# Kernel tuning notes

Hardware: AMD Instinct MI355X
Metric: run time of the kernel (lower is better)

## Reference

```python
import jax, jax.numpy as jnp
import numpy as np

N, E, D, L = 50000, 800000, 128, 2
EPS = 1e-7

def _logmap0(y):
    # Poincare ball (c=1) logmap at origin: artanh(||y||) * y / ||y||
    n = jnp.linalg.norm(y, axis=-1, keepdims=True)
    nc = jnp.clip(n, EPS, 1.0 - 1e-5)
    return jnp.arctanh(nc) * y / jnp.maximum(n, EPS)

def _expmap0(u):
    # Poincare ball (c=1) expmap at origin: tanh(||u||) * u / ||u||
    n = jnp.linalg.norm(u, axis=-1, keepdims=True)
    return jnp.tanh(n) * u / jnp.maximum(n, EPS)

def _l2norm(x):
    # F.normalize(p=2, dim=1)
    return x / jnp.maximum(jnp.linalg.norm(x, axis=1, keepdims=True), 1e-12)

def setup_inputs() -> dict:
    key = jax.random.key(0)
    ks = jax.random.split(key, 12)
    src = jax.random.randint(ks[0], (E,), 0, N)
    dst = jax.random.randint(ks[1], (E,), 0, N)
    e_emb = jax.random.normal(ks[2], (N, D), jnp.float32)
    b_emb = jax.random.normal(ks[3], (N, D), jnp.float32) * 0.1  # inside Poincare ball
    s_emb = jax.random.normal(ks[4], (N, D), jnp.float32)
    sc = 0.05
    eW = jax.random.normal(ks[5], (L, D, D), jnp.float32) * sc
    eB = jax.random.normal(ks[6], (L, D), jnp.float32) * sc
    bW = jax.random.normal(ks[7], (L, D, D), jnp.float32) * sc
    bB = jax.random.normal(ks[8], (L, D), jnp.float32) * sc
    sW = jax.random.normal(ks[9], (L, D, D), jnp.float32) * sc
    sB = jax.random.normal(ks[10], (L, D), jnp.float32) * sc
    return dict(e_emb=e_emb, b_emb=b_emb, s_emb=s_emb, eW=eW, eB=eB,
                bW=bW, bB=bB, sW=sW, sB=sB, src=src, dst=dst)

def reference(e_emb, b_emb, s_emb, eW, eB, bW, bB, sW, sB, src, dst):
    n_nodes = e_emb.shape[0]
    ones_e = jnp.ones(src.shape[0], jnp.float32)
    in_deg = jax.ops.segment_sum(ones_e, dst, num_segments=n_nodes)
    out_deg = jax.ops.segment_sum(ones_e, src, num_segments=n_nodes)
    # DGL GraphConv norm='both': D_out^{-1/2} (sum over in-neighbors) D_in^{-1/2}
    norm_out = jnp.where(out_deg > 0, out_deg ** -0.5, 0.0)[:, None]
    norm_in = jnp.where(in_deg > 0, in_deg ** -0.5, 0.0)[:, None]
    inv_in = jnp.where(in_deg > 0, 1.0 / in_deg, 0.0)[:, None]  # mean reduce

    def agg_sum(h):
        return jax.ops.segment_sum(h[src], dst, num_segments=n_nodes)

    for l in range(L):
        # Euclidean branch: GraphConv(norm='both') then LeakyReLU(0.2)
        h = agg_sum(e_emb * norm_out) * norm_in
        e_emb = jax.nn.leaky_relu(h @ eW[l].T + eB[l], negative_slope=0.2)
        # Hyperbolic branch: logmap0 -> Linear -> neighbor mean -> expmap0
        tan_b = _logmap0(b_emb) @ bW[l].T + bB[l]
        b_emb = _expmap0(agg_sum(tan_b) * inv_in)
        # Spherical branch: normalize -> Linear -> neighbor mean -> normalize
        tan_s = _l2norm(s_emb) @ sW[l].T + sB[l]
        s_emb = _l2norm(agg_sum(tan_s) * inv_in)
    return (e_emb, b_emb, s_emb)
```

## Files before the change

kernel.cpp:

```cpp
#include <hip/hip_runtime.h>
#include <math.h>

#define DD 128
#define PSTRIDE 384

typedef _Float16 half8 __attribute__((ext_vector_type(8)));
typedef float floatx4 __attribute__((ext_vector_type(4)));

__device__ __forceinline__ float g16_sum(float x) {
#pragma unroll
  for (int m = 8; m >= 1; m >>= 1) x += __shfl_xor(x, m, 64);
  return x;
}
__device__ __forceinline__ int wave_sum_i(int x) {
#pragma unroll
  for (int m = 32; m >= 1; m >>= 1) x += __shfl_xor(x, m, 64);
  return x;
}

__global__ void deg_wcvt_kernel(const int* __restrict__ src, const int* __restrict__ dst,
                                int* __restrict__ out_deg8, int* __restrict__ in_deg8,
                                int E, int N,
                                const float* __restrict__ eW, const float* __restrict__ bW,
                                const float* __restrict__ sW, _Float16* __restrict__ Wh, int nW,
                                int DB) {
  int bx = blockIdx.x;
  if (bx < DB) {
    int e = bx * 256 + threadIdx.x;
    if (e < E) {
      int h = ((bx << 2) + (threadIdx.x >> 6)) & 7;
      atomicAdd(&out_deg8[h * N + src[e]], 1);
      atomicAdd(&in_deg8[h * N + dst[e]], 1);
    }
  } else {
    int i = (bx - DB) * 256 + threadIdx.x;
    if (i < nW) {
      Wh[i]          = (_Float16)eW[i];
      Wh[i + nW]     = (_Float16)bW[i];
      Wh[i + 2 * nW] = (_Float16)sW[i];
    }
  }
}

__global__ void norms_psum_kernel(const int* __restrict__ in_deg8, const int* __restrict__ out_deg8,
                                  int* __restrict__ in_deg, float* __restrict__ norm_in,
                                  float* __restrict__ norm_out, float* __restrict__ inv_in,
                                  int* __restrict__ part, int N) {
  __shared__ int wsum[4];
  int t = threadIdx.x, lane = t & 63, w = t >> 6;
  int i = blockIdx.x * 256 + t;
  int di = 0;
  if (i < N) {
    int dq = 0;
#pragma unroll
    for (int h = 0; h < 8; ++h) {
      di += in_deg8[h * N + i];
      dq += out_deg8[h * N + i];
    }
    in_deg[i] = di;
    norm_in[i]  = di > 0 ? 1.0f / sqrtf((float)di) : 0.0f;
    norm_out[i] = dq > 0 ? 1.0f / sqrtf((float)dq) : 0.0f;
    inv_in[i]   = di > 0 ? 1.0f / (float)di : 0.0f;
  }
  int s = wave_sum_i(di);
  if (lane == 0) wsum[w] = s;
  __syncthreads();
  if (t == 0) part[blockIdx.x] = wsum[0] + wsum[1] + wsum[2] + wsum[3];
}

__global__ void part_scan_kernel(int* __restrict__ part, int nb) {
  __shared__ int wsum[4];
  int t = threadIdx.x, lane = t & 63, w = t >> 6;
  int x = (t < nb) ? part[t] : 0;
  int v = x;
#pragma unroll
  for (int off = 1; off < 64; off <<= 1) {
    int y = __shfl_up(v, off, 64);
    if (lane >= off) v += y;
  }
  if (lane == 63) wsum[w] = v;
  __syncthreads();
  int base = 0;
  for (int j = 0; j < w; ++j) base += wsum[j];
  if (t < nb) part[t] = base + v - x;
}

__global__ void local_scan_kernel(const int* __restrict__ deg, const int* __restrict__ part,
                                  int* __restrict__ row_off, int N, int E) {
  __shared__ int wsum[4];
  int t = threadIdx.x, lane = t & 63, w = t >> 6;
  int i = blockIdx.x * 256 + t;
  int x = (i < N) ? deg[i] : 0;
  int v = x;
#pragma unroll
  for (int off = 1; off < 64; off <<= 1) {
    int y = __shfl_up(v, off, 64);
    if (lane >= off) v += y;
  }
  if (lane == 63) wsum[w] = v;
  __syncthreads();
  int base = 0;
  for (int j = 0; j < w; ++j) base += wsum[j];
  if (i < N) row_off[i] = part[blockIdx.x] + base + v - x;
  if (blockIdx.x == 0 && t == 0) row_off[N] = E;
}

__device__ __forceinline__ void gemm0_tile(int part, int rb, const float* __restrict__ A,
                                           const _Float16* __restrict__ Wh,
                                           const float* __restrict__ Bb,
                                           _Float16* __restrict__ Q, int N) {
  int t = threadIdx.x, lane = t & 63, w = t >> 6;
  int m = lane & 15, quad = lane >> 4, c0 = w * 32;
  int rbase = rb * 64;
  _Float16* Qo = Q + part * DD;
  half8 bf[2][4];
#pragma unroll
  for (int tj = 0; tj < 2; ++tj)
#pragma unroll
    for (int kk = 0; kk < 4; ++kk)
      bf[tj][kk] = *(const half8*)&Wh[(c0 + tj * 16 + m) * DD + kk * 32 + quad * 8];
  float bias0 = 0.f, bias1 = 0.f;
  if (part) { bias0 = Bb[c0 + m]; bias1 = Bb[c0 + 16 + m]; }
#pragma unroll
  for (int r = 0; r < 4; ++r) {
    int row0 = r * 16;
    int arow = rbase + row0 + m; if (arow >= N) arow = N - 1;
    const float* Ap = A + (size_t)arow * DD;
    half8 af[4];
    float nsq = 0.f;
#pragma unroll
    for (int kk = 0; kk < 4; ++kk) {
      float4 x0 = *(const float4*)&Ap[kk * 32 + quad * 8];
      float4 x1 = *(const float4*)&Ap[kk * 32 + quad * 8 + 4];
      if (part)
        nsq += x0.x * x0.x + x0.y * x0.y + x0.z * x0.z + x0.w * x0.w +
               x1.x * x1.x + x1.y * x1.y + x1.z * x1.z + x1.w * x1.w;
      half8 a;
      a[0] = (_Float16)x0.x; a[1] = (_Float16)x0.y; a[2] = (_Float16)x0.z; a[3] = (_Float16)x0.w;
      a[4] = (_Float16)x1.x; a[5] = (_Float16)x1.y; a[6] = (_Float16)x1.z; a[7] = (_Float16)x1.w;
      af[kk] = a;
    }
    float fr = 1.f;
    if (part) {
      nsq += __shfl_xor(nsq, 16, 64);
      nsq += __shfl_xor(nsq, 32, 64);
      float n = sqrtf(nsq);
      if (part == 1) {
        float nc = fminf(fmaxf(n, 1e-7f), 1.0f - 1e-5f);
        fr = atanhf(nc) / fmaxf(n, 1e-7f);
      } else {
        fr = 1.0f / fmaxf(n, 1e-12f);
      }
    }
    floatx4 acc0 = {0.f, 0.f, 0.f, 0.f}, acc1 = {0.f, 0.f, 0.f, 0.f};
#pragma unroll
    for (int kk = 0; kk < 4; ++kk) {
      acc0 = __builtin_amdgcn_mfma_f32_16x16x32_f16(af[kk], bf[0][kk], acc0, 0, 0, 0);
      acc1 = __builtin_amdgcn_mfma_f32_16x16x32_f16(af[kk], bf[1][kk], acc1, 0, 0, 0);
    }
    int vrow = rbase + row0 + quad * 4;
#pragma unroll
    for (int reg = 0; reg < 4; ++reg) {
      int v = vrow + reg;
      float fs = part ? __shfl(fr, quad * 4 + reg, 64) : 1.f;
      if (v < N) {
        Qo[(size_t)v * PSTRIDE + c0 + m]      = (_Float16)(acc0[reg] * fs + bias0);
        Qo[(size_t)v * PSTRIDE + c0 + 16 + m] = (_Float16)(acc1[reg] * fs + bias1);
      }
    }
  }
}

__device__ __forceinline__ void gemm_tile(int part, int rb, const _Float16* __restrict__ P,
                                          const _Float16* __restrict__ Wh,
                                          const float* __restrict__ Bb,
                                          _Float16* __restrict__ Q, int N) {
  int t = threadIdx.x, lane = t & 63, w = t >> 6;
  int m = lane & 15, quad = lane >> 4, c0 = w * 32;
  int rbase = rb * 64;
  const _Float16* Ain = P + part * DD;
  _Float16* Qo = Q + part * DD;
  half8 bf[2][4];
#pragma unroll
  for (int tj = 0; tj < 2; ++tj)
#pragma unroll
    for (int kk = 0; kk < 4; ++kk)
      bf[tj][kk] = *(const half8*)&Wh[(c0 + tj * 16 + m) * DD + kk * 32 + quad * 8];
  float bias0 = 0.f, bias1 = 0.f;
  if (Bb) { bias0 = Bb[c0 + m]; bias1 = Bb[c0 + 16 + m]; }
#pragma unroll
  for (int r = 0; r < 4; ++r) {
    int row0 = r * 16;
    int arow = rbase + row0 + m; if (arow >= N) arow = N - 1;
    const _Float16* Ap = Ain + (size_t)arow * PSTRIDE;
    floatx4 acc0 = {0.f, 0.f, 0.f, 0.f}, acc1 = {0.f, 0.f, 0.f, 0.f};
#pragma unroll
    for (int kk = 0; kk < 4; ++kk) {
      half8 af = *(const half8*)&Ap[kk * 32 + quad * 8];
      acc0 = __builtin_amdgcn_mfma_f32_16x16x32_f16(af, bf[0][kk], acc0, 0, 0, 0);
      acc1 = __builtin_amdgcn_mfma_f32_16x16x32_f16(af, bf[1][kk], acc1, 0, 0, 0);
    }
    int vrow = rbase + row0 + quad * 4;
#pragma unroll
    for (int reg = 0; reg < 4; ++reg) {
      int v = vrow + reg;
      if (v < N) {
        Qo[(size_t)v * PSTRIDE + c0 + m]      = (_Float16)(acc0[reg] + bias0);
        Qo[(size_t)v * PSTRIDE + c0 + 16 + m] = (_Float16)(acc1[reg] + bias1);
      }
    }
  }
}

__global__ __launch_bounds__(256) void fill_gemm0_kernel(
    const int* __restrict__ src, const int* __restrict__ dst,
    const float* __restrict__ norm_out, const int* __restrict__ row_off,
    int* __restrict__ cursor, int2* __restrict__ csr_sw, int E,
    const float* __restrict__ e0, const float* __restrict__ b0, const float* __restrict__ s0,
    const _Float16* __restrict__ WhE, const _Float16* __restrict__ WhB,
    const _Float16* __restrict__ WhS, const float* __restrict__ bBl,
    const float* __restrict__ sBl, _Float16* __restrict__ Q, int N, int FB, int GB) {
  int bx = blockIdx.x;
  if (bx < FB) {
    int e = bx * 256 + threadIdx.x;
    if (e < E) {
      int d = dst[e], s = src[e];
      int pos = row_off[d] + atomicAdd(&cursor[d], 1);
      csr_sw[pos] = make_int2(s, __float_as_int(norm_out[s]));
    }
  } else {
    int gb = bx - FB;
    int part = gb / GB, rb = gb % GB;
    const float* A = (part == 0) ? e0 : (part == 1 ? b0 : s0);
    const _Float16* Wh = (part == 0) ? WhE : (part == 1 ? WhB : WhS);
    const float* Bb = (part == 0) ? nullptr : (part == 1 ? bBl : sBl);
    gemm0_tile(part, rb, A, Wh, Bb, Q, N);
  }
}

__global__ __launch_bounds__(256) void gemm3_kernel(const _Float16* __restrict__ P,
                                                    const _Float16* __restrict__ WhE,
                                                    const _Float16* __restrict__ WhB,
                                                    const _Float16* __restrict__ WhS,
                                                    const float* __restrict__ bBl,
                                                    const float* __restrict__ sBl,
                                                    _Float16* __restrict__ Q, int N) {
  int part = blockIdx.y;
  const _Float16* Wh = (part == 0) ? WhE : (part == 1 ? WhB : WhS);
  const float* Bb = (part == 0) ? nullptr : (part == 1 ? bBl : sBl);
  gemm_tile(part, blockIdx.x, P, Wh, Bb, Q, N);
}

__global__ __launch_bounds__(256) void agg_fused_kernel(
    const _Float16* __restrict__ Q, const int* __restrict__ row_off,
    const int2* __restrict__ csr_sw, const float* __restrict__ norm_in,
    const float* __restrict__ inv_in, const float* __restrict__ eBias,
    float* __restrict__ oe, float* __restrict__ ob, float* __restrict__ os,
    _Float16* __restrict__ Pnext, int N, int write_pack, int write_out) {
  int lane = threadIdx.x & 63;
  int v = blockIdx.x * 4 + (threadIdx.x >> 6);
  if (v >= N) return;
  int g = lane >> 4, q = lane & 15;
  int beg = row_off[v], end = row_off[v + 1];
  float eacc[8], bacc[8], sacc[8];
#pragma unroll
  for (int j = 0; j < 8; ++j) { eacc[j] = 0.f; bacc[j] = 0.f; sacc[j] = 0.f; }
  int i = beg;
  for (; i + 8 <= end; i += 8) {
    int2 swa = csr_sw[i + g];
    int2 swb = csr_sw[i + 4 + g];
    float wa = __int_as_float(swa.y), wb = __int_as_float(swb.y);
    const _Float16* ra = Q + (size_t)swa.x * PSTRIDE + q * 8;
    const _Float16* rb = Q + (size_t)swb.x * PSTRIDE + q * 8;
    half8 ea = *(const half8*)ra;
    half8 e2 = *(const half8*)rb;
    half8 ba = *(const half8*)(ra + 128);
    half8 b2 = *(const half8*)(rb + 128);
    half8 sa = *(const half8*)(ra + 256);
    half8 s2 = *(const half8*)(rb + 256);
#pragma unroll
    for (int j = 0; j < 8; ++j) {
      eacc[j] += wa * (float)ea[j];
      eacc[j] += wb * (float)e2[j];
      bacc[j] += (float)ba[j];
      bacc[j] += (float)b2[j];
      sacc[j] += (float)sa[j];
      sacc[j] += (float)s2[j];
    }
  }
  if (i + 4 <= end) {
    int2 sw = csr_sw[i + g];
    float wgt = __int_as_float(sw.y);
    const _Float16* rp = Q + (size_t)sw.x * PSTRIDE + q * 8;
    half8 ev = *(const half8*)rp;
    half8 bv = *(const half8*)(rp + 128);
    half8 sv = *(const half8*)(rp + 256);
#pragma unroll
    for (int j = 0; j < 8; ++j) {
      eacc[j] += wgt * (float)ev[j];
      bacc[j] += (float)bv[j];
      sacc[j] += (float)sv[j];
    }
    i += 4;
  }
  if (i + g < end) {
    int2 sw = csr_sw[i + g];
    float wgt = __int_as_float(sw.y);
    const _Float16* rp = Q + (size_t)sw.x * PSTRIDE + q * 8;
    half8 ev = *(const half8*)rp;
    half8 bv = *(const half8*)(rp + 128);
    half8 sv = *(const half8*)(rp + 256);
#pragma unroll
    for (int j = 0; j < 8; ++j) {
      eacc[j] += wgt * (float)ev[j];
      bacc[j] += (float)bv[j];
      sacc[j] += (float)sv[j];
    }
  }
#pragma unroll
  for (int j = 0; j < 8; ++j) {
    eacc[j] += __shfl_xor(eacc[j], 16, 64);
    eacc[j] += __shfl_xor(eacc[j], 32, 64);
    bacc[j] += __shfl_xor(bacc[j], 16, 64);
    bacc[j] += __shfl_xor(bacc[j], 32, 64);
    sacc[j] += __shfl_xor(sacc[j], 16, 64);
    sacc[j] += __shfl_xor(sacc[j], 32, 64);
  }
  float ni = norm_in[v], iv = inv_in[v];
  const float4* ebp = (const float4*)eBias;
  float4 eb0 = ebp[q * 2], eb1 = ebp[q * 2 + 1];
  float bias[8] = {eb0.x, eb0.y, eb0.z, eb0.w, eb1.x, eb1.y, eb1.z, eb1.w};
  float h[8], ub[8], us[8];
  float ss2 = 0.f;
#pragma unroll
  for (int j = 0; j < 8; ++j) {
    float t = eacc[j] * ni + bias[j];
    h[j] = t > 0.f ? t : 0.2f * t;
    ub[j] = bacc[j] * iv;
    us[j] = sacc[j] * iv; ss2 += us[j] * us[j];
  }
  float ns = sqrtf(g16_sum(ss2));
  float fs = 1.0f / fmaxf(ns, 1e-12f);
  if (write_out) {
    float bs2 = 0.f;
#pragma unroll
    for (int j = 0; j < 8; ++j) bs2 += ub[j] * ub[j];
    float nb = sqrtf(g16_sum(bs2));
    float fb = tanhf(nb) / fmaxf(nb, 1e-7f);
    if (g == 0) {
      float4* p = (float4*)(oe + (size_t)v * DD);
      p[q * 2]     = make_float4(h[0], h[1], h[2], h[3]);
      p[q * 2 + 1] = make_float4(h[4], h[5], h[6], h[7]);
    } else if (g == 1) {
      float4* p = (float4*)(ob + (size_t)v * DD);
      p[q * 2]     = make_float4(ub[0] * fb, ub[1] * fb, ub[2] * fb, ub[3] * fb);
      p[q * 2 + 1] = make_float4(ub[4] * fb, ub[5] * fb, ub[6] * fb, ub[7] * fb);
    } else if (g == 2) {
      float4* p = (float4*)(os + (size_t)v * DD);
      p[q * 2]     = make_float4(us[0] * fs, us[1] * fs, us[2] * fs, us[3] * fs);
      p[q * 2 + 1] = make_float4(us[4] * fs, us[5] * fs, us[6] * fs, us[7] * fs);
    }
  }
  if (write_pack) {
    if (g == 3) {
      half8 he, hb, hs;
#pragma unroll
      for (int j = 0; j < 8; ++j) {
        he[j] = (_Float16)h[j];
        hb[j] = (_Float16)ub[j];
        hs[j] = (_Float16)(us[j] * fs);
      }
      _Float16* Pr = Pnext + (size_t)v * PSTRIDE + q * 8;
      *(half8*)&Pr[0]   = he;
      *(half8*)&Pr[128] = hb;
      *(half8*)&Pr[256] = hs;
    }
  }
}

extern "C" void kernel_launch(void* const* d_in, const int* in_sizes, int n_in,
                              void* d_out, int out_size, void* d_ws, size_t ws_size,
                              hipStream_t stream) {
  const float* e0 = (const float*)d_in[0];
  const float* b0 = (const float*)d_in[1];
  const float* s0 = (const float*)d_in[2];
  const float* eW = (const float*)d_in[3];
  const float* eB = (const float*)d_in[4];
  const float* bW = (const float*)d_in[5];
  const float* bB = (const float*)d_in[6];
  const float* sW = (const float*)d_in[7];
  const float* sB = (const float*)d_in[8];
  const int* src = (const int*)d_in[9];
  const int* dst = (const int*)d_in[10];
  int N = in_sizes[0] / DD;
  int E = in_sizes[9];
  int L = in_sizes[3] / (DD * DD);
  int LDD2 = L * DD * DD;

  char* w = (char*)d_ws;
  int* in_deg8  = (int*)w; w += (size_t)8 * N * 4;
  int* out_deg8 = (int*)w; w += (size_t)8 * N * 4;
  int* cursor   = (int*)w; w += (size_t)N * 4;
  int* in_deg   = (int*)w; w += (size_t)N * 4;
  int* row_off  = (int*)w; w += (size_t)(N + 4) * 4;
  int* pscan    = (int*)w; w += (size_t)1024 * 4;
  int2* csr_sw  = (int2*)w; w += (size_t)E * 8;
  float* norm_in  = (float*)w; w += (size_t)N * 4;
  float* norm_out = (float*)w; w += (size_t)N * 4;
  float* inv_in   = (float*)w; w += (size_t)N * 4;
  w = (char*)(((size_t)w + 255) & ~(size_t)255);
  _Float16* P = (_Float16*)w; w += (size_t)N * PSTRIDE * 2;
  _Float16* Q = (_Float16*)w; w += (size_t)N * PSTRIDE * 2;
  _Float16* Wh = (_Float16*)w; w += (size_t)3 * LDD2 * 2;
  _Float16* whE = Wh;
  _Float16* whB = Wh + LDD2;
  _Float16* whS = Wh + 2 * LDD2;

  float* oe = (float*)d_out;
  float* ob = oe + (size_t)N * DD;
  float* os = ob + (size_t)N * DD;

  int DB = (E + 255) / 256;
  int AB = (N + 3) / 4;
  int GB = (N + 63) / 64;
  int WB = (LDD2 + 255) / 256;
  int PB = (N + 255) / 256;

  hipMemsetAsync(d_ws, 0, (size_t)17 * N * 4, stream);
  deg_wcvt_kernel<<<DB + WB, 256, 0, stream>>>(src, dst, out_deg8, in_deg8, E, N,
                                               eW, bW, sW, Wh, LDD2, DB);
  norms_psum_kernel<<<PB, 256, 0, stream>>>(in_deg8, out_deg8, in_deg,
                                            norm_in, norm_out, inv_in, pscan, N);
  part_scan_kernel<<<1, 256, 0, stream>>>(pscan, PB);
  local_scan_kernel<<<PB, 256, 0, stream>>>(in_deg, pscan, row_off, N, E);
  fill_gemm0_kernel<<<DB + 3 * GB, 256, 0, stream>>>(src, dst, norm_out, row_off, cursor,
                                                     csr_sw, E, e0, b0, s0,
                                                     whE, whB, whS, bB, sB, Q, N, DB, GB);
  agg_fused_kernel<<<AB, 256, 0, stream>>>(Q, row_off, csr_sw, norm_in, inv_in, eB,
                                           oe, ob, os, P, N,
                                           (L > 1) ? 1 : 0, (L == 1) ? 1 : 0);
  for (int l = 1; l < L; ++l) {
    size_t lo = (size_t)l * DD * DD;
    gemm3_kernel<<<dim3(GB, 3), 256, 0, stream>>>(P, whE + lo, whB + lo, whS + lo,
                                                  bB + (size_t)l * DD, sB + (size_t)l * DD, Q, N);
    agg_fused_kernel<<<AB, 256, 0, stream>>>(Q, row_off, csr_sw, norm_in, inv_in,
                                             eB + (size_t)l * DD, oe, ob, os, P, N,
                                             (l < L - 1) ? 1 : 0, (l == L - 1) ? 1 : 0);
  }
}
```

Before: 494.2 us.

## Capture in-degree atomic ranks to drop cursor atomics in CSR fill

The in-degree histogram atomics now record each edge's return value as a per-bin rank. The local scan turns the 8 per-bin counts into exclusive bin offsets. The CSR fill then computes each slot directly from bin offset plus rank, removing the second round of atomics on a cursor array. The cost is an extra E-sized rank buffer written and read back, and the bin index changes from a per-wavefront value to e&7.

```diff
diff --git a/kernel.cpp b/kernel.cpp
--- a/kernel.cpp
+++ b/kernel.cpp
@@ -20,7 +20,7 @@
 
 __global__ void deg_wcvt_kernel(const int* __restrict__ src, const int* __restrict__ dst,
                                 int* __restrict__ out_deg8, int* __restrict__ in_deg8,
-                                int E, int N,
+                                int* __restrict__ rank8, int E, int N,
                                 const float* __restrict__ eW, const float* __restrict__ bW,
                                 const float* __restrict__ sW, _Float16* __restrict__ Wh, int nW,
                                 int DB) {
@@ -28,9 +28,9 @@
   if (bx < DB) {
     int e = bx * 256 + threadIdx.x;
     if (e < E) {
-      int h = ((bx << 2) + (threadIdx.x >> 6)) & 7;
+      int h = e & 7;
       atomicAdd(&out_deg8[h * N + src[e]], 1);
-      atomicAdd(&in_deg8[h * N + dst[e]], 1);
+      rank8[e] = atomicAdd(&in_deg8[h * N + dst[e]], 1);
     }
   } else {
     int i = (bx - DB) * 256 + threadIdx.x;
@@ -86,7 +86,8 @@
 }
 
 __global__ void local_scan_kernel(const int* __restrict__ deg, const int* __restrict__ part,
-                                  int* __restrict__ row_off, int N, int E) {
+                                  int* __restrict__ row_off, int* __restrict__ in_deg8,
+                                  int N, int E) {
   __shared__ int wsum[4];
   int t = threadIdx.x, lane = t & 63, w = t >> 6;
   int i = blockIdx.x * 256 + t;
@@ -101,7 +102,17 @@
   __syncthreads();
   int base = 0;
   for (int j = 0; j < w; ++j) base += wsum[j];
-  if (i < N) row_off[i] = part[blockIdx.x] + base + v - x;
+  if (i < N) {
+    int ro = part[blockIdx.x] + base + v - x;
+    row_off[i] = ro;
+    int cum = ro;
+#pragma unroll
+    for (int h = 0; h < 8; ++h) {
+      int c = in_deg8[h * N + i];
+      in_deg8[h * N + i] = cum;
+      cum += c;
+    }
+  }
   if (blockIdx.x == 0 && t == 0) row_off[N] = E;
 }
 
@@ -214,8 +225,8 @@
 
 __global__ __launch_bounds__(256) void fill_gemm0_kernel(
     const int* __restrict__ src, const int* __restrict__ dst,
-    const float* __restrict__ norm_out, const int* __restrict__ row_off,
-    int* __restrict__ cursor, int2* __restrict__ csr_sw, int E,
+    const int* __restrict__ rank8, const int* __restrict__ bin_base,
+    const float* __restrict__ norm_out, int2* __restrict__ csr_sw, int E,
     const float* __restrict__ e0, const float* __restrict__ b0, const float* __restrict__ s0,
     const _Float16* __restrict__ WhE, const _Float16* __restrict__ WhB,
     const _Float16* __restrict__ WhS, const float* __restrict__ bBl,
@@ -225,7 +236,8 @@
     int e = bx * 256 + threadIdx.x;
     if (e < E) {
       int d = dst[e], s = src[e];
-      int pos = row_off[d] + atomicAdd(&cursor[d], 1);
+      int h = e & 7;
+      int pos = bin_base[h * N + d] + rank8[e];
       csr_sw[pos] = make_int2(s, __float_as_int(norm_out[s]));
     }
   } else {
@@ -400,7 +412,7 @@
   char* w = (char*)d_ws;
   int* in_deg8  = (int*)w; w += (size_t)8 * N * 4;
   int* out_deg8 = (int*)w; w += (size_t)8 * N * 4;
-  int* cursor   = (int*)w; w += (size_t)N * 4;
+  int* rank8    = (int*)w; w += (size_t)E * 4;
   int* in_deg   = (int*)w; w += (size_t)N * 4;
   int* row_off  = (int*)w; w += (size_t)(N + 4) * 4;
   int* pscan    = (int*)w; w += (size_t)1024 * 4;
@@ -426,14 +438,14 @@
   int WB = (LDD2 + 255) / 256;
   int PB = (N + 255) / 256;
 
-  hipMemsetAsync(d_ws, 0, (size_t)17 * N * 4, stream);
-  deg_wcvt_kernel<<<DB + WB, 256, 0, stream>>>(src, dst, out_deg8, in_deg8, E, N,
+  hipMemsetAsync(d_ws, 0, (size_t)16 * N * 4, stream);
+  deg_wcvt_kernel<<<DB + WB, 256, 0, stream>>>(src, dst, out_deg8, in_deg8, rank8, E, N,
                                                eW, bW, sW, Wh, LDD2, DB);
   norms_psum_kernel<<<PB, 256, 0, stream>>>(in_deg8, out_deg8, in_deg,
                                             norm_in, norm_out, inv_in, pscan, N);
   part_scan_kernel<<<1, 256, 0, stream>>>(pscan, PB);
-  local_scan_kernel<<<PB, 256, 0, stream>>>(in_deg, pscan, row_off, N, E);
-  fill_gemm0_kernel<<<DB + 3 * GB, 256, 0, stream>>>(src, dst, norm_out, row_off, cursor,
+  local_scan_kernel<<<PB, 256, 0, stream>>>(in_deg, pscan, row_off, in_deg8, N, E);
+  fill_gemm0_kernel<<<DB + 3 * GB, 256, 0, stream>>>(src, dst, rank8, in_deg8, norm_out,
                                                      csr_sw, E, e0, b0, s0,
                                                      whE, whB, whS, bB, sB, Q, N, DB, GB);
   agg_fused_kernel<<<AB, 256, 0, stream>>>(Q, row_off, csr_sw, norm_in, inv_in, eB,
```

New measurement: 482.2 us. 1.02x faster.
